# Kernel tuning notes

Measured on AMD Instinct MI355X. Metric: run time of the kernel, lower is better.

## Reference

```python
import jax, jax.numpy as jnp
import numpy as np

B, S, H = 1, 2048, 1024
E, F, K = 8, 3584, 2


def setup_inputs() -> dict:
    key = jax.random.key(0)
    ks = jax.random.split(key, 5)
    scale_h = 1.0 / np.sqrt(H)
    scale_f = 1.0 / np.sqrt(F)
    return {
        "hidden_states": jax.random.normal(ks[0], (B, S, H), dtype=jnp.float32),
        "gate_w": jax.random.normal(ks[1], (E, H), dtype=jnp.float32) * scale_h,
        "w1": jax.random.normal(ks[2], (E, F, H), dtype=jnp.float32) * scale_h,
        "w2": jax.random.normal(ks[3], (E, H, F), dtype=jnp.float32) * scale_f,
        "w3": jax.random.normal(ks[4], (E, F, H), dtype=jnp.float32) * scale_h,
    }


def reference(hidden_states, gate_w, w1, w2, w3):
    b, s, h = hidden_states.shape
    x = hidden_states.reshape(-1, h)                      # [T, H]
    T = x.shape[0]
    router_logits = x @ gate_w.T                          # [T, E]
    probs = jax.nn.softmax(router_logits.astype(jnp.float32), axis=-1)
    rw, sel = jax.lax.top_k(probs, K)                     # [T, K]
    rw = rw / jnp.sum(rw, axis=-1, keepdims=True)
    rw = rw.astype(x.dtype)
    # combine weights per (token, expert): scatter top-k routing weights
    combine = jnp.zeros((T, E), dtype=x.dtype).at[
        jnp.arange(T)[:, None], sel
    ].add(rw)                                             # [T, E]
    out = jnp.zeros_like(x)
    for e in range(E):  # small fixed expert count
        # SwiGLU expert FFN (F.linear: x @ W.T)
        hmid = jax.nn.silu(x @ w1[e].T) * (x @ w3[e].T)   # [T, F]
        out = out + combine[:, e:e + 1] * (hmid @ w2[e].T)
    return out.reshape(b, s, h), router_logits
```

## Files before the change

### kernel.cpp

```cpp
#include <hip/hip_runtime.h>
#include <hip/hip_bf16.h>
#include <math.h>

namespace {
constexpr int kT = 2048;
constexpr int kH = 1024;
constexpr int kE = 8;
constexpr int kF = 3584;
constexpr int kK = 2;

constexpr size_t OFF_CNT  = 0;
constexpr size_t OFF_LIST = 1024;
constexpr size_t OFF_RW   = OFF_LIST + sizeof(int) * kE * kT;
constexpr size_t OFF_HMID = 1u << 20;

typedef __attribute__((ext_vector_type(8))) short bf16x8;
typedef __attribute__((ext_vector_type(4))) float fx4;
}

__device__ __forceinline__ short f2bf_s(float f) {
  union { __hip_bfloat16 h; short s; } u;
  u.h = __float2bfloat16(f);
  return u.s;
}

__device__ __forceinline__ bf16x8 pack8(float4 a, float4 b) {
  bf16x8 r;
  r[0] = f2bf_s(a.x); r[1] = f2bf_s(a.y);
  r[2] = f2bf_s(a.z); r[3] = f2bf_s(a.w);
  r[4] = f2bf_s(b.x); r[5] = f2bf_s(b.y);
  r[6] = f2bf_s(b.z); r[7] = f2bf_s(b.w);
  return r;
}

__device__ __forceinline__ int swz(int row, int u) {
  return row * 64 + ((u ^ (row & 7)) << 3);
}

__global__ __launch_bounds__(256) void router_kernel(
    const float* __restrict__ x, const float* __restrict__ gw,
    float* __restrict__ logits_out, int* __restrict__ cnt,
    int* __restrict__ list, float* __restrict__ rw) {
  const int t = blockIdx.x;
  const float* xt = x + (size_t)t * kH;
  __shared__ float lg[kE];
  const int wave = threadIdx.x >> 6;
  const int lane = threadIdx.x & 63;
  for (int e = wave; e < kE; e += 4) {
    const float* g = gw + (size_t)e * kH;
    float s = 0.f;
    for (int h = lane; h < kH; h += 64) s += xt[h] * g[h];
#pragma unroll
    for (int off = 32; off > 0; off >>= 1) s += __shfl_down(s, off, 64);
    if (lane == 0) lg[e] = s;
  }
  __syncthreads();
  if (threadIdx.x < kE) logits_out[(size_t)t * kE + threadIdx.x] = lg[threadIdx.x];
  if (threadIdx.x == 0) {
    float m = lg[0];
#pragma unroll
    for (int e = 1; e < kE; ++e) m = fmaxf(m, lg[e]);
    float p[kE];
#pragma unroll
    for (int e = 0; e < kE; ++e) p[e] = expf(lg[e] - m);
    int i0 = 0;
#pragma unroll
    for (int e = 1; e < kE; ++e) if (p[e] > p[i0]) i0 = e;
    int i1 = (i0 == 0) ? 1 : 0;
#pragma unroll
    for (int e = 0; e < kE; ++e)
      if (e != i0 && e != i1 && p[e] > p[i1]) i1 = e;
    const float w0 = p[i0], w1v = p[i1];
    const float inv = 1.f / (w0 + w1v);
    rw[t * kK + 0] = w0 * inv;
    rw[t * kK + 1] = w1v * inv;
    const int s0 = atomicAdd(&cnt[i0], 1);
    list[i0 * kT + s0] = t * kK + 0;
    const int s1 = atomicAdd(&cnt[i1], 1);
    list[i1 * kT + s1] = t * kK + 1;
  }
}

__global__ __launch_bounds__(256) void moe_mid_mfma(
    const float* __restrict__ x, const float* __restrict__ w1,
    const float* __restrict__ w3, const int* __restrict__ cnt,
    const int* __restrict__ list, unsigned short* __restrict__ hmid) {
  const int e = blockIdx.z;
  const int n = cnt[e];
  const int t0 = blockIdx.y * 128;
  if (t0 >= n) return;
  const int f0 = blockIdx.x * 64;

  __shared__ short As[2][128 * 64];
  __shared__ short B1s[2][64 * 64];
  __shared__ short B3s[2][64 * 64];
  __shared__ int ppid[128];
  __shared__ int ptok[128];

  const int tid = threadIdx.x;
  if (tid < 128) {
    const int idx = t0 + tid;
    const int pid = (idx < n) ? list[e * kT + idx] : -1;
    ppid[tid] = pid;
    ptok[tid] = (pid < 0) ? 0 : (pid >> 1);
  }
  __syncthreads();

  const float* w1e = w1 + (size_t)e * kF * kH;
  const float* w3e = w3 + (size_t)e * kF * kH;

  const float* a_src[4];
  int a_sw[4];
#pragma unroll
  for (int i = 0; i < 4; ++i) {
    const int flat = tid + 256 * i;
    const int row = flat >> 3, u = flat & 7;
    a_src[i] = x + (size_t)ptok[row] * kH + u * 8;
    a_sw[i] = swz(row, u);
  }
  const int brow = tid >> 2, bup = tid & 3;
  const float* b1_src = w1e + (size_t)(f0 + brow) * kH + bup * 16;
  const float* b3_src = w3e + (size_t)(f0 + brow) * kH + bup * 16;
  const int b_sw0 = swz(brow, 2 * bup), b_sw1 = swz(brow, 2 * bup + 1);

  const int lane = tid & 63, wid = tid >> 6;
  const int wr = wid >> 1, wc = wid & 1;
  const int lr = lane & 15, lq = lane >> 4;

  fx4 acc1[4][2], acc3[4][2];
#pragma unroll
  for (int i = 0; i < 4; ++i)
#pragma unroll
    for (int j = 0; j < 2; ++j) { acc1[i][j] = (fx4)(0.f); acc3[i][j] = (fx4)(0.f); }

  float4 aR[4][2], b1R[4], b3R[4];
  auto LOAD = [&](int k0) {
#pragma unroll
    for (int i = 0; i < 4; ++i) {
      aR[i][0] = *reinterpret_cast<const float4*>(a_src[i] + k0);
      aR[i][1] = *reinterpret_cast<const float4*>(a_src[i] + k0 + 4);
    }
#pragma unroll
    for (int j = 0; j < 4; ++j) {
      b1R[j] = *reinterpret_cast<const float4*>(b1_src + k0 + j * 4);
      b3R[j] = *reinterpret_cast<const float4*>(b3_src + k0 + j * 4);
    }
  };
  auto STORE = [&](int buf) {
    short* Ab = As[buf]; short* B1b = B1s[buf]; short* B3b = B3s[buf];
#pragma unroll
    for (int i = 0; i < 4; ++i)
      *reinterpret_cast<bf16x8*>(&Ab[a_sw[i]]) = pack8(aR[i][0], aR[i][1]);
    *reinterpret_cast<bf16x8*>(&B1b[b_sw0]) = pack8(b1R[0], b1R[1]);
    *reinterpret_cast<bf16x8*>(&B1b[b_sw1]) = pack8(b1R[2], b1R[3]);
    *reinterpret_cast<bf16x8*>(&B3b[b_sw0]) = pack8(b3R[0], b3R[1]);
    *reinterpret_cast<bf16x8*>(&B3b[b_sw1]) = pack8(b3R[2], b3R[3]);
  };

  LOAD(0); STORE(0); __syncthreads();
  int cur = 0;
  constexpr int NIT = kH / 64;
  for (int it = 0; it < NIT; ++it) {
    const bool pf = (it + 1 < NIT);
    if (pf) LOAD((it + 1) * 64);
    const short* Ab = As[cur]; const short* B1b = B1s[cur]; const short* B3b = B3s[cur];
    __builtin_amdgcn_s_setprio(1);
#pragma unroll
    for (int ks = 0; ks < 2; ++ks) {
      bf16x8 a[4], bb1[2], bb3[2];
#pragma unroll
      for (int mi = 0; mi < 4; ++mi)
        a[mi] = *reinterpret_cast<const bf16x8*>(&Ab[swz(wr * 64 + mi * 16 + lr, ks * 4 + lq)]);
#pragma unroll
      for (int ni = 0; ni < 2; ++ni) {
        bb1[ni] = *reinterpret_cast<const bf16x8*>(&B1b[swz(wc * 32 + ni * 16 + lr, ks * 4 + lq)]);
        bb3[ni] = *reinterpret_cast<const bf16x8*>(&B3b[swz(wc * 32 + ni * 16 + lr, ks * 4 + lq)]);
      }
#pragma unroll
      for (int mi = 0; mi < 4; ++mi)
#pragma unroll
        for (int ni = 0; ni < 2; ++ni) {
          acc1[mi][ni] = __builtin_amdgcn_mfma_f32_16x16x32_bf16(a[mi], bb1[ni], acc1[mi][ni], 0, 0, 0);
          acc3[mi][ni] = __builtin_amdgcn_mfma_f32_16x16x32_bf16(a[mi], bb3[ni], acc3[mi][ni], 0, 0, 0);
        }
    }
    __builtin_amdgcn_s_setprio(0);
    if (pf) STORE(cur ^ 1);
    __syncthreads();
    cur ^= 1;
  }

#pragma unroll
  for (int mi = 0; mi < 4; ++mi)
#pragma unroll
    for (int i = 0; i < 4; ++i) {
      const int row = wr * 64 + mi * 16 + lq * 4 + i;
      const int pid = ppid[row];
      if (pid < 0) continue;
#pragma unroll
      for (int ni = 0; ni < 2; ++ni) {
        const int col = f0 + wc * 32 + ni * 16 + lr;
        const float s1 = acc1[mi][ni][i];
        const float s3 = acc3[mi][ni][i];
        const float h = s1 * s3 / (1.f + expf(-s1));
        hmid[(size_t)pid * kF + col] = (unsigned short)f2bf_s(h);
      }
    }
}

__global__ __launch_bounds__(256) void moe_out_mfma(
    const unsigned short* __restrict__ hmid, const float* __restrict__ w2,
    const int* __restrict__ cnt, const int* __restrict__ list,
    const float* __restrict__ rw, float* __restrict__ out) {
  const int e = blockIdx.z;
  const int n = cnt[e];
  const int p0 = blockIdx.y * 128;
  if (p0 >= n) return;
  const int h0 = blockIdx.x * 64;

  __shared__ short As[2][128 * 64];
  __shared__ short Bs[2][64 * 64];
  __shared__ int ppid[128];
  __shared__ int prow[128];

  const int tid = threadIdx.x;
  if (tid < 128) {
    const int idx = p0 + tid;
    const int pid = (idx < n) ? list[e * kT + idx] : -1;
    ppid[tid] = pid;
    prow[tid] = (pid < 0) ? 0 : pid;
  }
  __syncthreads();

  const float* w2e = w2 + (size_t)e * kH * kF;

  const unsigned short* a_src[4];
  int a_sw[4];
#pragma unroll
  for (int i = 0; i < 4; ++i) {
    const int flat = tid + 256 * i;
    const int row = flat >> 3, u = flat & 7;
    a_src[i] = hmid + (size_t)prow[row] * kF + u * 8;
    a_sw[i] = swz(row, u);
  }
  const int brow = tid >> 2, bup = tid & 3;
  const float* b_src = w2e + (size_t)(h0 + brow) * kF + bup * 16;
  const int b_sw0 = swz(brow, 2 * bup), b_sw1 = swz(brow, 2 * bup + 1);

  const int lane = tid & 63, wid = tid >> 6;
  const int wr = wid >> 1, wc = wid & 1;
  const int lr = lane & 15, lq = lane >> 4;

  fx4 acc[4][2];
#pragma unroll
  for (int i = 0; i < 4; ++i)
#pragma unroll
    for (int j = 0; j < 2; ++j) acc[i][j] = (fx4)(0.f);

  bf16x8 aR[4];
  float4 bR[4];
  auto LOAD = [&](int k0) {
#pragma unroll
    for (int i = 0; i < 4; ++i)
      aR[i] = *reinterpret_cast<const bf16x8*>(a_src[i] + k0);
#pragma unroll
    for (int j = 0; j < 4; ++j)
      bR[j] = *reinterpret_cast<const float4*>(b_src + k0 + j * 4);
  };
  auto STORE = [&](int buf) {
    short* Ab = As[buf]; short* Bb = Bs[buf];
#pragma unroll
    for (int i = 0; i < 4; ++i)
      *reinterpret_cast<bf16x8*>(&Ab[a_sw[i]]) = aR[i];
    *reinterpret_cast<bf16x8*>(&Bb[b_sw0]) = pack8(bR[0], bR[1]);
    *reinterpret_cast<bf16x8*>(&Bb[b_sw1]) = pack8(bR[2], bR[3]);
  };

  LOAD(0); STORE(0); __syncthreads();
  int cur = 0;
  constexpr int NIT = kF / 64;
  for (int it = 0; it < NIT; ++it) {
    const bool pf = (it + 1 < NIT);
    if (pf) LOAD((it + 1) * 64);
    const short* Ab = As[cur]; const short* Bb = Bs[cur];
    __builtin_amdgcn_s_setprio(1);
#pragma unroll
    for (int ks = 0; ks < 2; ++ks) {
      bf16x8 a[4], b[2];
#pragma unroll
      for (int mi = 0; mi < 4; ++mi)
        a[mi] = *reinterpret_cast<const bf16x8*>(&Ab[swz(wr * 64 + mi * 16 + lr, ks * 4 + lq)]);
#pragma unroll
      for (int ni = 0; ni < 2; ++ni)
        b[ni] = *reinterpret_cast<const bf16x8*>(&Bb[swz(wc * 32 + ni * 16 + lr, ks * 4 + lq)]);
#pragma unroll
      for (int mi = 0; mi < 4; ++mi)
#pragma unroll
        for (int ni = 0; ni < 2; ++ni)
          acc[mi][ni] = __builtin_amdgcn_mfma_f32_16x16x32_bf16(a[mi], b[ni], acc[mi][ni], 0, 0, 0);
    }
    __builtin_amdgcn_s_setprio(0);
    if (pf) STORE(cur ^ 1);
    __syncthreads();
    cur ^= 1;
  }

#pragma unroll
  for (int mi = 0; mi < 4; ++mi)
#pragma unroll
    for (int i = 0; i < 4; ++i) {
      const int row = wr * 64 + mi * 16 + lq * 4 + i;
      const int pid = ppid[row];
      if (pid < 0) continue;
      const int tok = pid >> 1;
      const float w = rw[pid];
      float* op = out + (size_t)tok * kH + h0 + wc * 32 + lr;
#pragma unroll
      for (int ni = 0; ni < 2; ++ni)
        atomicAdd(&op[ni * 16], w * acc[mi][ni][i]);
    }
}

extern "C" void kernel_launch(void* const* d_in, const int* in_sizes, int n_in,
                              void* d_out, int out_size, void* d_ws,
                              size_t ws_size, hipStream_t stream) {
  (void)in_sizes; (void)n_in; (void)out_size; (void)ws_size;
  const float* x  = (const float*)d_in[0];
  const float* gw = (const float*)d_in[1];
  const float* w1 = (const float*)d_in[2];
  const float* w2 = (const float*)d_in[3];
  const float* w3 = (const float*)d_in[4];

  float* out    = (float*)d_out;
  float* logits = out + (size_t)kT * kH;

  char* ws = (char*)d_ws;
  int*            cnt  = (int*)(ws + OFF_CNT);
  int*            list = (int*)(ws + OFF_LIST);
  float*          rw   = (float*)(ws + OFF_RW);
  unsigned short* hmid = (unsigned short*)(ws + OFF_HMID);

  hipMemsetAsync(out, 0, (size_t)kT * kH * sizeof(float), stream);
  hipMemsetAsync(cnt, 0, kE * sizeof(int), stream);

  router_kernel<<<kT, 256, 0, stream>>>(x, gw, logits, cnt, list, rw);

  dim3 g1(kF / 64, kT / 128, kE);
  moe_mid_mfma<<<g1, 256, 0, stream>>>(x, w1, w3, cnt, list, hmid);

  dim3 g2(kH / 64, kT / 128, kE);
  moe_out_mfma<<<g2, 256, 0, stream>>>(hmid, w2, cnt, list, rw, out);
}
```

Before: 342.4 us.

## Halve token tile to 64, add two-stage register prefetch, raise occupancy hints

Both expert GEMM kernels now use 64-token tiles instead of 128, which halves the accumulators and shared memory per block and doubles the grid. Launch-bound hints request 3 and 4 blocks per CU. The global-to-register prefetch goes from one stage ahead to two, using alternating register stages so loads overlap further with MFMA work. The B-tile load mapping is unified with the A mapping (8 elements per thread per row chunk). The cost is that each weight tile is now re-read from global memory twice as often, since more token tiles per expert each load it, which adds memory traffic.

```diff
diff --git a/kernel.cpp b/kernel.cpp
--- a/kernel.cpp
+++ b/kernel.cpp
@@ -81,24 +81,26 @@
   }
 }
 
-__global__ __launch_bounds__(256) void moe_mid_mfma(
+struct StageM { float4 a[2][2], b1[2][2], b3[2][2]; };
+
+__global__ __launch_bounds__(256, 3) void moe_mid_mfma(
     const float* __restrict__ x, const float* __restrict__ w1,
     const float* __restrict__ w3, const int* __restrict__ cnt,
     const int* __restrict__ list, unsigned short* __restrict__ hmid) {
   const int e = blockIdx.z;
   const int n = cnt[e];
-  const int t0 = blockIdx.y * 128;
+  const int t0 = blockIdx.y * 64;
   if (t0 >= n) return;
   const int f0 = blockIdx.x * 64;
 
-  __shared__ short As[2][128 * 64];
+  __shared__ short As[2][64 * 64];
   __shared__ short B1s[2][64 * 64];
   __shared__ short B3s[2][64 * 64];
-  __shared__ int ppid[128];
-  __shared__ int ptok[128];
+  __shared__ int ppid[64];
+  __shared__ int ptok[64];
 
   const int tid = threadIdx.x;
-  if (tid < 128) {
+  if (tid < 64) {
     const int idx = t0 + tid;
     const int pid = (idx < n) ? list[e * kT + idx] : -1;
     ppid[tid] = pid;
@@ -109,75 +111,63 @@
   const float* w1e = w1 + (size_t)e * kF * kH;
   const float* w3e = w3 + (size_t)e * kF * kH;
 
-  const float* a_src[4];
-  int a_sw[4];
-#pragma unroll
-  for (int i = 0; i < 4; ++i) {
+  const float* a_src[2]; const float* b1_src[2]; const float* b3_src[2];
+  int sw_[2];
+#pragma unroll
+  for (int i = 0; i < 2; ++i) {
     const int flat = tid + 256 * i;
     const int row = flat >> 3, u = flat & 7;
-    a_src[i] = x + (size_t)ptok[row] * kH + u * 8;
-    a_sw[i] = swz(row, u);
-  }
-  const int brow = tid >> 2, bup = tid & 3;
-  const float* b1_src = w1e + (size_t)(f0 + brow) * kH + bup * 16;
-  const float* b3_src = w3e + (size_t)(f0 + brow) * kH + bup * 16;
-  const int b_sw0 = swz(brow, 2 * bup), b_sw1 = swz(brow, 2 * bup + 1);
+    a_src[i]  = x + (size_t)ptok[row] * kH + u * 8;
+    b1_src[i] = w1e + (size_t)(f0 + row) * kH + u * 8;
+    b3_src[i] = w3e + (size_t)(f0 + row) * kH + u * 8;
+    sw_[i] = swz(row, u);
+  }
 
   const int lane = tid & 63, wid = tid >> 6;
   const int wr = wid >> 1, wc = wid & 1;
   const int lr = lane & 15, lq = lane >> 4;
 
-  fx4 acc1[4][2], acc3[4][2];
-#pragma unroll
-  for (int i = 0; i < 4; ++i)
+  fx4 acc1[2][2], acc3[2][2];
+#pragma unroll
+  for (int i = 0; i < 2; ++i)
 #pragma unroll
     for (int j = 0; j < 2; ++j) { acc1[i][j] = (fx4)(0.f); acc3[i][j] = (fx4)(0.f); }
 
-  float4 aR[4][2], b1R[4], b3R[4];
-  auto LOAD = [&](int k0) {
-#pragma unroll
-    for (int i = 0; i < 4; ++i) {
-      aR[i][0] = *reinterpret_cast<const float4*>(a_src[i] + k0);
-      aR[i][1] = *reinterpret_cast<const float4*>(a_src[i] + k0 + 4);
-    }
-#pragma unroll
-    for (int j = 0; j < 4; ++j) {
-      b1R[j] = *reinterpret_cast<const float4*>(b1_src + k0 + j * 4);
-      b3R[j] = *reinterpret_cast<const float4*>(b3_src + k0 + j * 4);
-    }
-  };
-  auto STORE = [&](int buf) {
-    short* Ab = As[buf]; short* B1b = B1s[buf]; short* B3b = B3s[buf];
-#pragma unroll
-    for (int i = 0; i < 4; ++i)
-      *reinterpret_cast<bf16x8*>(&Ab[a_sw[i]]) = pack8(aR[i][0], aR[i][1]);
-    *reinterpret_cast<bf16x8*>(&B1b[b_sw0]) = pack8(b1R[0], b1R[1]);
-    *reinterpret_cast<bf16x8*>(&B1b[b_sw1]) = pack8(b1R[2], b1R[3]);
-    *reinterpret_cast<bf16x8*>(&B3b[b_sw0]) = pack8(b3R[0], b3R[1]);
-    *reinterpret_cast<bf16x8*>(&B3b[b_sw1]) = pack8(b3R[2], b3R[3]);
-  };
-
-  LOAD(0); STORE(0); __syncthreads();
-  int cur = 0;
-  constexpr int NIT = kH / 64;
-  for (int it = 0; it < NIT; ++it) {
-    const bool pf = (it + 1 < NIT);
-    if (pf) LOAD((it + 1) * 64);
-    const short* Ab = As[cur]; const short* B1b = B1s[cur]; const short* B3b = B3s[cur];
+  auto LOAD = [&](StageM& S, int k0) {
+#pragma unroll
+    for (int i = 0; i < 2; ++i) {
+      S.a[i][0]  = *reinterpret_cast<const float4*>(a_src[i] + k0);
+      S.a[i][1]  = *reinterpret_cast<const float4*>(a_src[i] + k0 + 4);
+      S.b1[i][0] = *reinterpret_cast<const float4*>(b1_src[i] + k0);
+      S.b1[i][1] = *reinterpret_cast<const float4*>(b1_src[i] + k0 + 4);
+      S.b3[i][0] = *reinterpret_cast<const float4*>(b3_src[i] + k0);
+      S.b3[i][1] = *reinterpret_cast<const float4*>(b3_src[i] + k0 + 4);
+    }
+  };
+  auto STORE = [&](const StageM& S, int buf) {
+#pragma unroll
+    for (int i = 0; i < 2; ++i) {
+      *reinterpret_cast<bf16x8*>(&As[buf][sw_[i]])  = pack8(S.a[i][0], S.a[i][1]);
+      *reinterpret_cast<bf16x8*>(&B1s[buf][sw_[i]]) = pack8(S.b1[i][0], S.b1[i][1]);
+      *reinterpret_cast<bf16x8*>(&B3s[buf][sw_[i]]) = pack8(S.b3[i][0], S.b3[i][1]);
+    }
+  };
+  auto MFMA_PHASE = [&](int buf) {
+    const short* Ab = As[buf]; const short* B1b = B1s[buf]; const short* B3b = B3s[buf];
     __builtin_amdgcn_s_setprio(1);
 #pragma unroll
     for (int ks = 0; ks < 2; ++ks) {
-      bf16x8 a[4], bb1[2], bb3[2];
-#pragma unroll
-      for (int mi = 0; mi < 4; ++mi)
-        a[mi] = *reinterpret_cast<const bf16x8*>(&Ab[swz(wr * 64 + mi * 16 + lr, ks * 4 + lq)]);
+      bf16x8 a[2], bb1[2], bb3[2];
+#pragma unroll
+      for (int mi = 0; mi < 2; ++mi)
+        a[mi] = *reinterpret_cast<const bf16x8*>(&Ab[swz(wr * 32 + mi * 16 + lr, ks * 4 + lq)]);
 #pragma unroll
       for (int ni = 0; ni < 2; ++ni) {
         bb1[ni] = *reinterpret_cast<const bf16x8*>(&B1b[swz(wc * 32 + ni * 16 + lr, ks * 4 + lq)]);
         bb3[ni] = *reinterpret_cast<const bf16x8*>(&B3b[swz(wc * 32 + ni * 16 + lr, ks * 4 + lq)]);
       }
 #pragma unroll
-      for (int mi = 0; mi < 4; ++mi)
+      for (int mi = 0; mi < 2; ++mi)
 #pragma unroll
         for (int ni = 0; ni < 2; ++ni) {
           acc1[mi][ni] = __builtin_amdgcn_mfma_f32_16x16x32_bf16(a[mi], bb1[ni], acc1[mi][ni], 0, 0, 0);
@@ -185,16 +175,33 @@
         }
     }
     __builtin_amdgcn_s_setprio(0);
-    if (pf) STORE(cur ^ 1);
+  };
+
+  StageM R0, R1;
+  constexpr int NIT = kH / 64;
+  LOAD(R0, 0);
+  LOAD(R1, 64);
+  STORE(R0, 0);
+  __syncthreads();
+#pragma unroll 2
+  for (int it = 0; it < NIT; ++it) {
+    if (it & 1) {
+      if (it + 2 < NIT) LOAD(R1, (it + 2) * 64);
+      MFMA_PHASE(1);
+      if (it + 1 < NIT) STORE(R0, 0);
+    } else {
+      if (it + 2 < NIT) LOAD(R0, (it + 2) * 64);
+      MFMA_PHASE(0);
+      if (it + 1 < NIT) STORE(R1, 1);
+    }
     __syncthreads();
-    cur ^= 1;
-  }
-
-#pragma unroll
-  for (int mi = 0; mi < 4; ++mi)
+  }
+
+#pragma unroll
+  for (int mi = 0; mi < 2; ++mi)
 #pragma unroll
     for (int i = 0; i < 4; ++i) {
-      const int row = wr * 64 + mi * 16 + lq * 4 + i;
+      const int row = wr * 32 + mi * 16 + lq * 4 + i;
       const int pid = ppid[row];
       if (pid < 0) continue;
 #pragma unroll
@@ -208,23 +215,25 @@
     }
 }
 
-__global__ __launch_bounds__(256) void moe_out_mfma(
+struct StageO { bf16x8 a[2]; float4 b[2][2]; };
+
+__global__ __launch_bounds__(256, 4) void moe_out_mfma(
     const unsigned short* __restrict__ hmid, const float* __restrict__ w2,
     const int* __restrict__ cnt, const int* __restrict__ list,
     const float* __restrict__ rw, float* __restrict__ out) {
   const int e = blockIdx.z;
   const int n = cnt[e];
-  const int p0 = blockIdx.y * 128;
+  const int p0 = blockIdx.y * 64;
   if (p0 >= n) return;
   const int h0 = blockIdx.x * 64;
 
-  __shared__ short As[2][128 * 64];
+  __shared__ short As[2][64 * 64];
   __shared__ short Bs[2][64 * 64];
-  __shared__ int ppid[128];
-  __shared__ int prow[128];
+  __shared__ int ppid[64];
+  __shared__ int prow[64];
 
   const int tid = threadIdx.x;
-  if (tid < 128) {
+  if (tid < 64) {
     const int idx = p0 + tid;
     const int pid = (idx < n) ? list[e * kT + idx] : -1;
     ppid[tid] = pid;
@@ -234,82 +243,88 @@
 
   const float* w2e = w2 + (size_t)e * kH * kF;
 
-  const unsigned short* a_src[4];
-  int a_sw[4];
-#pragma unroll
-  for (int i = 0; i < 4; ++i) {
+  const unsigned short* a_src[2]; const float* b_src[2];
+  int sw_[2];
+#pragma unroll
+  for (int i = 0; i < 2; ++i) {
     const int flat = tid + 256 * i;
     const int row = flat >> 3, u = flat & 7;
     a_src[i] = hmid + (size_t)prow[row] * kF + u * 8;
-    a_sw[i] = swz(row, u);
-  }
-  const int brow = tid >> 2, bup = tid & 3;
-  const float* b_src = w2e + (size_t)(h0 + brow) * kF + bup * 16;
-  const int b_sw0 = swz(brow, 2 * bup), b_sw1 = swz(brow, 2 * bup + 1);
+    b_src[i] = w2e + (size_t)(h0 + row) * kF + u * 8;
+    sw_[i] = swz(row, u);
+  }
 
   const int lane = tid & 63, wid = tid >> 6;
   const int wr = wid >> 1, wc = wid & 1;
   const int lr = lane & 15, lq = lane >> 4;
 
-  fx4 acc[4][2];
-#pragma unroll
-  for (int i = 0; i < 4; ++i)
+  fx4 acc[2][2];
+#pragma unroll
+  for (int i = 0; i < 2; ++i)
 #pragma unroll
     for (int j = 0; j < 2; ++j) acc[i][j] = (fx4)(0.f);
 
-  bf16x8 aR[4];
-  float4 bR[4];
-  auto LOAD = [&](int k0) {
-#pragma unroll
-    for (int i = 0; i < 4; ++i)
-      aR[i] = *reinterpret_cast<const bf16x8*>(a_src[i] + k0);
-#pragma unroll
-    for (int j = 0; j < 4; ++j)
-      bR[j] = *reinterpret_cast<const float4*>(b_src + k0 + j * 4);
-  };
-  auto STORE = [&](int buf) {
-    short* Ab = As[buf]; short* Bb = Bs[buf];
-#pragma unroll
-    for (int i = 0; i < 4; ++i)
-      *reinterpret_cast<bf16x8*>(&Ab[a_sw[i]]) = aR[i];
-    *reinterpret_cast<bf16x8*>(&Bb[b_sw0]) = pack8(bR[0], bR[1]);
-    *reinterpret_cast<bf16x8*>(&Bb[b_sw1]) = pack8(bR[2], bR[3]);
-  };
-
-  LOAD(0); STORE(0); __syncthreads();
-  int cur = 0;
-  constexpr int NIT = kF / 64;
-  for (int it = 0; it < NIT; ++it) {
-    const bool pf = (it + 1 < NIT);
-    if (pf) LOAD((it + 1) * 64);
-    const short* Ab = As[cur]; const short* Bb = Bs[cur];
+  auto LOAD = [&](StageO& S, int k0) {
+#pragma unroll
+    for (int i = 0; i < 2; ++i) {
+      S.a[i]    = *reinterpret_cast<const bf16x8*>(a_src[i] + k0);
+      S.b[i][0] = *reinterpret_cast<const float4*>(b_src[i] + k0);
+      S.b[i][1] = *reinterpret_cast<const float4*>(b_src[i] + k0 + 4);
+    }
+  };
+  auto STORE = [&](const StageO& S, int buf) {
+#pragma unroll
+    for (int i = 0; i < 2; ++i) {
+      *reinterpret_cast<bf16x8*>(&As[buf][sw_[i]]) = S.a[i];
+      *reinterpret_cast<bf16x8*>(&Bs[buf][sw_[i]]) = pack8(S.b[i][0], S.b[i][1]);
+    }
+  };
+  auto MFMA_PHASE = [&](int buf) {
+    const short* Ab = As[buf]; const short* Bb = Bs[buf];
     __builtin_amdgcn_s_setprio(1);
 #pragma unroll
     for (int ks = 0; ks < 2; ++ks) {
-      bf16x8 a[4], b[2];
-#pragma unroll
-      for (int mi = 0; mi < 4; ++mi)
-        a[mi] = *reinterpret_cast<const bf16x8*>(&Ab[swz(wr * 64 + mi * 16 + lr, ks * 4 + lq)]);
+      bf16x8 a[2], b[2];
+#pragma unroll
+      for (int mi = 0; mi < 2; ++mi)
+        a[mi] = *reinterpret_cast<const bf16x8*>(&Ab[swz(wr * 32 + mi * 16 + lr, ks * 4 + lq)]);
 #pragma unroll
       for (int ni = 0; ni < 2; ++ni)
         b[ni] = *reinterpret_cast<const bf16x8*>(&Bb[swz(wc * 32 + ni * 16 + lr, ks * 4 + lq)]);
 #pragma unroll
-      for (int mi = 0; mi < 4; ++mi)
+      for (int mi = 0; mi < 2; ++mi)
 #pragma unroll
         for (int ni = 0; ni < 2; ++ni)
           acc[mi][ni] = __builtin_amdgcn_mfma_f32_16x16x32_bf16(a[mi], b[ni], acc[mi][ni], 0, 0, 0);
     }
     __builtin_amdgcn_s_setprio(0);
-    if (pf) STORE(cur ^ 1);
+  };
+
+  StageO R0, R1;
+  constexpr int NIT = kF / 64;
+  LOAD(R0, 0);
+  LOAD(R1, 64);
+  STORE(R0, 0);
+  __syncthreads();
+#pragma unroll 2
+  for (int it = 0; it < NIT; ++it) {
+    if (it & 1) {
+      if (it + 2 < NIT) LOAD(R1, (it + 2) * 64);
+      MFMA_PHASE(1);
+      if (it + 1 < NIT) STORE(R0, 0);
+    } else {
+      if (it + 2 < NIT) LOAD(R0, (it + 2) * 64);
+      MFMA_PHASE(0);
+      if (it + 1 < NIT) STORE(R1, 1);
+    }
     __syncthreads();
-    cur ^= 1;
-  }
-
-#pragma unroll
-  for (int mi = 0; mi < 4; ++mi)
+  }
+
+#pragma unroll
+  for (int mi = 0; mi < 2; ++mi)
 #pragma unroll
     for (int i = 0; i < 4; ++i) {
-      const int row = wr * 64 + mi * 16 + lq * 4 + i;
+      const int row = wr * 32 + mi * 16 + lq * 4 + i;
       const int pid = ppid[row];
       if (pid < 0) continue;
       const int tok = pid >> 1;
@@ -345,9 +360,9 @@
 
   router_kernel<<<kT, 256, 0, stream>>>(x, gw, logits, cnt, list, rw);
 
-  dim3 g1(kF / 64, kT / 128, kE);
+  dim3 g1(kF / 64, kT / 64, kE);
   moe_mid_mfma<<<g1, 256, 0, stream>>>(x, w1, w3, cnt, list, hmid);
 
-  dim3 g2(kH / 64, kT / 128, kE);
+  dim3 g2(kH / 64, kT / 64, kE);
   moe_out_mfma<<<g2, 256, 0, stream>>>(hmid, w2, cnt, list, rw, out);
 }
```

After: 493.3 us. 1.44x slower.
